# Performance work log

Hardware: AMD Instinct MI355X
Metric: run time of the kernel (lower is better)

## Reference

```python
import jax, jax.numpy as jnp
import numpy as np

H = 128   # d_model / features
N = 32    # kept complex modes (d_state=64 -> 32 conjugate pairs)
B = 8
L = 8192


def setup_inputs() -> dict:
    key = jax.random.key(0)
    ks = jax.random.split(key, 8)
    x = jax.random.normal(ks[0], (B, H, L), jnp.float32)
    # S4D (diagonal SSM) kernel parameters; channels=2 for bidirectional
    C_re = (jax.random.normal(ks[1], (2, H, N), jnp.float32) * (0.5 ** 0.5))
    C_im = (jax.random.normal(ks[2], (2, H, N), jnp.float32) * (0.5 ** 0.5))
    log_A_real = jnp.log(0.5 * jnp.ones((H, N), jnp.float32))          # S4D-Lin init
    A_imag = jnp.tile(np.pi * jnp.arange(N, dtype=jnp.float32), (H, 1))
    # log_dt uniform in [log(1e-3), log(1e-1)]
    u = jax.random.uniform(ks[3], (H,), jnp.float32)
    log_dt = u * (np.log(0.1) - np.log(0.001)) + np.log(0.001)
    D = jax.random.normal(ks[4], (H,), jnp.float32)                    # skip term
    W_pw = jax.random.normal(ks[5], (H, H), jnp.float32) / np.sqrt(H)  # 1x1 conv weight (out, in)
    gamma = jnp.ones((H,), jnp.float32)
    beta = jnp.zeros((H,), jnp.float32)
    return {"x": x, "C_re": C_re, "C_im": C_im, "log_A_real": log_A_real,
            "A_imag": A_imag, "log_dt": log_dt, "D": D, "W_pw": W_pw,
            "gamma": gamma, "beta": beta}


def reference(x, C_re, C_im, log_A_real, A_imag, log_dt, D, W_pw, gamma, beta):
    Lx = x.shape[-1]
    # ---- S4D SSM kernel via Vandermonde (ZOH discretization) ----
    A = -jnp.exp(log_A_real) + 1j * A_imag                 # (H, N) complex
    dt = jnp.exp(log_dt)[:, None]                          # (H, 1)
    dtA = A * dt                                           # (H, N)
    C = C_re + 1j * C_im                                   # (2, H, N)
    Kc = C * ((jnp.exp(dtA) - 1.0) / A)                    # (2, H, N)
    vand = jnp.exp(dtA[:, :, None] * jnp.arange(Lx))       # (H, N, L)
    k = 2.0 * jnp.einsum('chn,hnl->chl', Kc, vand).real    # (2, H, L)
    # ---- bidirectional: causal half + anticausal (flipped) half ----
    k_full = (jnp.pad(k[0], ((0, 0), (0, Lx)))
              + jnp.pad(k[1][:, ::-1], ((0, 0), (Lx, 0))))  # (H, 2L)
    # ---- FFT convolution ----
    n = 2 * Lx
    y = jnp.fft.irfft(jnp.fft.rfft(x, n=n) * jnp.fft.rfft(k_full, n=n), n=n)[..., :Lx]
    y = y + x * D[:, None]                                 # skip connection
    y = jax.nn.gelu(y, approximate=False)                  # FFTConv default activation
    # ---- pointwise 1x1 conv (no bias) ----
    y = jnp.einsum('bhl,oh->bol', y, W_pw)
    # ---- BatchNorm1d (training-mode batch statistics) ----
    mean = jnp.mean(y, axis=(0, 2), keepdims=True)
    var = jnp.var(y, axis=(0, 2), keepdims=True)
    y = (y - mean) * jax.lax.rsqrt(var + 1e-5) * gamma[:, None] + beta[:, None]
    # ---- ELU + residual (dropout p=0) ----
    return jax.nn.elu(y) + x
```

## Files before the change

### kernel.cpp

```cpp
#include <hip/hip_runtime.h>
#include <math.h>

#define HCH   128
#define NMODE 32
#define BB    8
#define LLEN  8192
#define LC    256
#define CCH   (LLEN / LC)
#define ROWS  (BB * HCH)

typedef unsigned int uint;
typedef _Float16 f16x8 __attribute__((ext_vector_type(8)));
typedef float    f32x4 __attribute__((ext_vector_type(4)));

static __device__ __forceinline__ uint pk2(float a, float b) {
    union { _Float16 h[2]; uint u; } v;
    v.h[0] = (_Float16)a; v.h[1] = (_Float16)b;
    return v.u;
}

__device__ __forceinline__ float gelu_f(float y) {
    float z = fabsf(y) * 0.7071067811865476f;
    float p = fmaf(z, 0.078108f, 0.000972f);
    p = fmaf(z, p, 0.230389f);
    p = fmaf(z, p, 0.278393f);
    p = fmaf(z, p, 1.0f);
    float p2 = p * p;
    float p4 = p2 * p2;
    float er = 1.f - __builtin_amdgcn_rcpf(p4);
    float s  = copysignf(er, y);
    return 0.5f * y * (1.f + s);
}

#define DPP_ADD(v, ctrl) { int _t = __builtin_amdgcn_update_dpp(0, __float_as_int(v), \
                             (ctrl), 0xF, 0xF, true); (v) += __int_as_float(_t); }

__global__ __launch_bounds__(256) void k_prep(const float* __restrict__ C_re,
                                              const float* __restrict__ C_im,
                                              const float* __restrict__ logA,
                                              const float* __restrict__ Aim,
                                              const float* __restrict__ logdt,
                                              _Float16* __restrict__ aT,
                                              _Float16* __restrict__ eT,
                                              float* __restrict__ Pw,
                                              float* __restrict__ stats) {
    __shared__ float2 PL[32 * 257];
    __shared__ float4 G01[32];
    __shared__ float4 HG[32];
    __shared__ float2 WL[32];
    __shared__ float k0L[256], k1L[256];
    int tid  = threadIdx.x;
    int h    = blockIdx.x >> 1;
    int half = blockIdx.x & 1;
    if (blockIdx.x == 0) stats[tid] = 0.f;
    if (tid < 32) {
        int n = tid, idx = h * 32 + n;
        float ar = expf(logA[idx]);
        float ai = Aim[idx];
        float dt = expf(logdt[h]);
        float dre = -ar * dt, dim = ai * dt;
        float er = expf(dre);
        float wr = er * cosf(dim), wi = er * sinf(dim);
        WL[n] = (float2){wr, wi};
        if (half == 0) {
            float eL = expf(dre * 256.f);
            Pw[idx]        = eL * cosf(dim * 256.f);
            Pw[4096 + idx] = eL * sinf(dim * 256.f);
        }
        float den  = ar * ar + ai * ai;
        float numr = -(wr - 1.f) * ar + wi * ai;
        float numi = -wi * ar - (wr - 1.f) * ai;
        float Kr = numr / den, Ki = numi / den;
        float c0r = C_re[idx],        c0i = C_im[idx];
        float c1r = C_re[4096 + idx], c1i = C_im[4096 + idx];
        float g0r = 2.f * (c0r * Kr - c0i * Ki), g0i = 2.f * (c0r * Ki + c0i * Kr);
        float g1r = 2.f * (c1r * Kr - c1i * Ki);
        float g1i = 2.f * (c1r * Ki + c1i * Kr);
        G01[n] = (float4){g0r, g0i, g1r, g1i};
        HG[n]  = (float4){g0r * wr - g0i * wi, g0r * wi + g0i * wr, g1r, g1i};
    }
    __syncthreads();
    {
        int n = tid & 31, tg = tid >> 5;
        float2 w = WL[n];
        float w2r = w.x * w.x - w.y * w.y,   w2i = 2.f * w.x * w.y;
        float w4r = w2r * w2r - w2i * w2i,   w4i = 2.f * w2r * w2i;
        float w8r = w4r * w4r - w4i * w4i,   w8i = 2.f * w4r * w4i;
        float pr = (tg & 1) ? w.x : 1.f;
        float pi = (tg & 1) ? w.y : 0.f;
        if (tg & 2) { float t2 = pr * w2r - pi * w2i; pi = pr * w2i + pi * w2r; pr = t2; }
        if (tg & 4) { float t4 = pr * w4r - pi * w4i; pi = pr * w4i + pi * w4r; pr = t4; }
        float2* row = &PL[n * 257];
        #pragma unroll
        for (int j = 0; j < 32; j++) {
            row[tg + 8 * j] = (float2){pr, pi};
            float tr = pr * w8r - pi * w8i; pi = pr * w8i + pi * w8r; pr = tr;
        }
    }
    __syncthreads();
    {
        int tau = tid;
        float s0 = 0.f, s1 = 0.f;
        #pragma unroll
        for (int n = 0; n < 32; n++) {
            float2 p = PL[n * 257 + tau];
            float4 g = G01[n];
            s0 += g.x * p.x - g.y * p.y;
            s1 += g.z * p.x - g.w * p.y;
        }
        k0L[tau] = s0; k1L[tau] = s1;
    }
    __syncthreads();
    #pragma unroll 4
    for (int i = 0; i < 64; i++) {
        int idx = i * 256 + tid;
        int t  = half * 128 + (idx >> 7);
        int sp = (idx & 127) << 1;
        float v0 = (sp     <= t) ? k0L[t - sp]     : k1L[sp - t - 1];
        float v1 = (sp + 1 <= t) ? k0L[t - sp - 1] : k1L[sp - t];
        *(uint*)&aT[((size_t)(h * 256 + t)) * 384 + sp] = pk2(v0, v1);
    }
    #pragma unroll 4
    for (int i = 0; i < 16; i++) {
        int idx = i * 256 + tid;
        int n = idx & 31;
        int t = half * 128 + (idx >> 5);
        float2 pt = PL[n * 257 + t];
        float2 pu = PL[n * 257 + 255 - t];
        float4 hg = HG[n];
        size_t rb = ((size_t)(h * 256 + t)) * 384;
        *(uint*)&aT[rb + 256 + 2 * n] = pk2(hg.x * pt.x - hg.y * pt.y,
                                            -(hg.x * pt.y + hg.y * pt.x));
        *(uint*)&aT[rb + 320 + 2 * n] = pk2(hg.z * pu.x - hg.w * pu.y,
                                            -(hg.z * pu.y + hg.w * pu.x));
    }
    #pragma unroll 4
    for (int i = 0; i < 16; i++) {
        int idx = i * 256 + tid;
        int n = idx >> 7;
        int s = half * 128 + (idx & 127);
        float2 ps = PL[n * 257 + s];
        float2 pu = PL[n * 257 + 255 - s];
        size_t base = (size_t)h * 128 * 256;
        eT[base + (size_t)(2 * n) * 256 + s]      = (_Float16)pu.x;
        eT[base + (size_t)(2 * n + 1) * 256 + s]  = (_Float16)pu.y;
        eT[base + (size_t)(64 + 2 * n) * 256 + s] = (_Float16)ps.x;
        eT[base + (size_t)(65 + 2 * n) * 256 + s] = (_Float16)ps.y;
    }
}

__global__ __launch_bounds__(256, 2) void k_states_g(const float* __restrict__ x,
                                                     const _Float16* __restrict__ eT,
                                                     float* __restrict__ S_end) {
    __shared__ _Float16 At[128 * 40];
    __shared__ _Float16 Bt[128 * 40];
    int tid = threadIdx.x;
    int bid = blockIdx.x;
    int h = bid >> 1, mt = bid & 1;
    int wave = tid >> 6, lane = tid & 63;
    int wm = wave >> 1, wn = wave & 1;
    int lrow = lane & 15, quad = lane >> 4;
    int koff = quad * 8;
    f32x4 acc[4][4];
    #pragma unroll
    for (int a = 0; a < 4; a++)
        #pragma unroll
        for (int b = 0; b < 4; b++) acc[a][b] = (f32x4){0.f, 0.f, 0.f, 0.f};

    for (int kk = 0; kk < 256; kk += 32) {
        __syncthreads();
        #pragma unroll
        for (int i = 0; i < 4; i++) {
            int idx = tid + i * 256;
            int r = idx >> 3, seg = idx & 7;
            int bc = mt * 128 + r;
            const float* xp = x + (((size_t)((bc >> 5) * HCH + h)) << 13) + ((bc & 31) << 8) + kk + seg * 4;
            float4 v = *(const float4*)xp;
            uint2 o; o.x = pk2(v.x, v.y); o.y = pk2(v.z, v.w);
            *(uint2*)&At[r * 40 + seg * 4] = o;
        }
        #pragma unroll
        for (int i = 0; i < 2; i++) {
            int idx = tid + i * 256;
            int r = idx >> 2, sg = idx & 3;
            uint4 v = *(const uint4*)(eT + ((size_t)(h * 128 + r)) * 256 + kk + sg * 8);
            *(uint4*)&Bt[r * 40 + sg * 8] = v;
        }
        __syncthreads();
        f16x8 a[4], b[4];
        #pragma unroll
        for (int f = 0; f < 4; f++) {
            a[f] = *(const f16x8*)&At[(wm * 64 + f * 16 + lrow) * 40 + koff];
            b[f] = *(const f16x8*)&Bt[(wn * 64 + f * 16 + lrow) * 40 + koff];
        }
        #pragma unroll
        for (int fi = 0; fi < 4; fi++)
            #pragma unroll
            for (int fj = 0; fj < 4; fj++)
                acc[fi][fj] = __builtin_amdgcn_mfma_f32_16x16x32_f16(a[fi], b[fj], acc[fi][fj], 0, 0, 0);
    }
    #pragma unroll
    for (int fi = 0; fi < 4; fi++) {
        #pragma unroll
        for (int fj = 0; fj < 4; fj++) {
            int srow = wn * 64 + fj * 16 + lrow;
            #pragma unroll
            for (int rg = 0; rg < 4; rg++) {
                int bc = mt * 128 + wm * 64 + fi * 16 + quad * 4 + rg;
                S_end[((size_t)(h * 256 + bc)) * 128 + srow] = acc[fi][fj][rg];
            }
        }
    }
}

__global__ void k_carries(const float* __restrict__ S_end, const float* __restrict__ Pw,
                          _Float16* __restrict__ carr) {
    int i = blockIdx.x * 256 + threadIdx.x;
    int n = i & 31; int d = (i >> 5) & 1; int row = i >> 6;
    int h = row & (HCH - 1), b = row >> 7;
    int pi = h * NMODE + n;
    float wLr = Pw[pi], wLi = Pw[4096 + pi];
    int srow = d * 64 + 2 * n;
    float cr = 0.f, ci = 0.f;
    if (d == 0) {
        for (int c = 0; c < CCH; c++) {
            size_t base = ((size_t)(h * 256 + b * 32 + c)) * 128 + srow;
            carr[base] = (_Float16)cr; carr[base + 1] = (_Float16)ci;
            float sr = S_end[base], si = S_end[base + 1];
            float nr = fmaf(wLr, cr, -wLi * ci) + sr;
            float ni = fmaf(wLi, cr,  wLr * ci) + si;
            cr = nr; ci = ni;
        }
    } else {
        for (int c = CCH - 1; c >= 0; c--) {
            size_t base = ((size_t)(h * 256 + b * 32 + c)) * 128 + srow;
            carr[base] = (_Float16)cr; carr[base + 1] = (_Float16)ci;
            float sr = S_end[base], si = S_end[base + 1];
            float nr = fmaf(wLr, cr, -wLi * ci) + sr;
            float ni = fmaf(wLi, cr,  wLr * ci) + si;
            cr = nr; ci = ni;
        }
    }
}

__global__ __launch_bounds__(256, 2) void k_conv_g(const float* __restrict__ x,
                                                   const _Float16* __restrict__ aT,
                                                   const _Float16* __restrict__ carr,
                                                   const float* __restrict__ D,
                                                   _Float16* __restrict__ Yg) {
    __shared__ _Float16 At[128 * 40];
    __shared__ _Float16 Bt[128 * 40];
    int tid = threadIdx.x;
    int bid = blockIdx.x;
    int h = bid >> 2, mt = (bid >> 1) & 1, nt = bid & 1;
    int wave = tid >> 6, lane = tid & 63;
    int wm = wave >> 1, wn = wave & 1;
    int lrow = lane & 15, quad = lane >> 4;
    int koff = quad * 8;
    f32x4 acc[4][4];
    #pragma unroll
    for (int a = 0; a < 4; a++)
        #pragma unroll
        for (int b = 0; b < 4; b++) acc[a][b] = (f32x4){0.f, 0.f, 0.f, 0.f};

    for (int kk = 0; kk < 384; kk += 32) {
        __syncthreads();
        if (kk < 256) {
            #pragma unroll
            for (int i = 0; i < 4; i++) {
                int idx = tid + i * 256;
                int r = idx >> 3, seg = idx & 7;
                int bc = mt * 128 + r;
                const float* xp = x + (((size_t)((bc >> 5) * HCH + h)) << 13) + ((bc & 31) << 8) + kk + seg * 4;
                float4 v = *(const float4*)xp;
                uint2 o; o.x = pk2(v.x, v.y); o.y = pk2(v.z, v.w);
                *(uint2*)&At[r * 40 + seg * 4] = o;
            }
        } else {
            #pragma unroll
            for (int i = 0; i < 2; i++) {
                int idx = tid + i * 256;
                int r = idx >> 2, sg = idx & 3;
                int bc = mt * 128 + r;
                uint4 v = *(const uint4*)(carr + ((size_t)(h * 256 + bc)) * 128 + (kk - 256) + sg * 8);
                *(uint4*)&At[r * 40 + sg * 8] = v;
            }
        }
        #pragma unroll
        for (int i = 0; i < 2; i++) {
            int idx = tid + i * 256;
            int r = idx >> 2, sg = idx & 3;
            int t = nt * 128 + r;
            uint4 v = *(const uint4*)(aT + ((size_t)(h * 256 + t)) * 384 + kk + sg * 8);
            *(uint4*)&Bt[r * 40 + sg * 8] = v;
        }
        __syncthreads();
        f16x8 a[4], b[4];
        #pragma unroll
        for (int f = 0; f < 4; f++) {
            a[f] = *(const f16x8*)&At[(wm * 64 + f * 16 + lrow) * 40 + koff];
            b[f] = *(const f16x8*)&Bt[(wn * 64 + f * 16 + lrow) * 40 + koff];
        }
        #pragma unroll
        for (int fi = 0; fi < 4; fi++)
            #pragma unroll
            for (int fj = 0; fj < 4; fj++)
                acc[fi][fj] = __builtin_amdgcn_mfma_f32_16x16x32_f16(a[fi], b[fj], acc[fi][fj], 0, 0, 0);
    }
    float Dh = D[h];
    #pragma unroll
    for (int fi = 0; fi < 4; fi++) {
        #pragma unroll
        for (int fj = 0; fj < 4; fj++) {
            int t = nt * 128 + wn * 64 + fj * 16 + lrow;
            #pragma unroll
            for (int rg = 0; rg < 4; rg++) {
                int bc = mt * 128 + wm * 64 + fi * 16 + quad * 4 + rg;
                size_t base = (((size_t)((bc >> 5) * HCH + h)) << 13) + ((bc & 31) << 8) + t;
                float xv = x[base];
                float yv = acc[fi][fj][rg] + Dh * xv;
                Yg[base] = (_Float16)gelu_f(yv);
            }
        }
    }
}

__global__ __launch_bounds__(256, 2) void k_pointwise(const _Float16* __restrict__ Yg,
                                                      const float* __restrict__ W,
                                                      float* __restrict__ z,
                                                      float* __restrict__ stats) {
    __shared__ _Float16 Wt[128 * 40];
    __shared__ _Float16 Yt[128 * 40];
    int tid = threadIdx.x;
    int b  = blockIdx.x >> 6;
    int l0 = (blockIdx.x & 63) << 7;
    int wave = tid >> 6, lane = tid & 63;
    int wm = wave >> 1, wn = wave & 1;
    int lrow = lane & 15, quad = lane >> 4;
    int koff = quad * 8;
    f32x4 acc[4][4];
    #pragma unroll
    for (int a = 0; a < 4; a++)
        #pragma unroll
        for (int c = 0; c < 4; c++) acc[a][c] = (f32x4){0.f, 0.f, 0.f, 0.f};

    for (int kk = 0; kk < 128; kk += 32) {
        __syncthreads();
        #pragma unroll
        for (int i = 0; i < 4; i++) {
            int idx = tid + i * 256;
            int r = idx >> 3, seg = idx & 7;
            float4 v = *(const float4*)(W + r * HCH + kk + seg * 4);
            uint2 o2; o2.x = pk2(v.x, v.y); o2.y = pk2(v.z, v.w);
            *(uint2*)&Wt[r * 40 + seg * 4] = o2;
        }
        #pragma unroll
        for (int i = 0; i < 2; i++) {
            int idx = tid + i * 256;
            int hh = idx & 31, lg = idx >> 5;
            uint4 v = *(const uint4*)(Yg + (((size_t)(b * HCH + kk + hh)) << 13) + l0 + lg * 8);
            const _Float16* hv = (const _Float16*)&v;
            #pragma unroll
            for (int j = 0; j < 8; j++)
                Yt[(lg * 8 + j) * 40 + hh] = hv[j];
        }
        __syncthreads();
        f16x8 a[4], bf[4];
        #pragma unroll
        for (int f = 0; f < 4; f++) {
            a[f]  = *(const f16x8*)&Wt[(wm * 64 + f * 16 + lrow) * 40 + koff];
            bf[f] = *(const f16x8*)&Yt[(wn * 64 + f * 16 + lrow) * 40 + koff];
        }
        #pragma unroll
        for (int fi = 0; fi < 4; fi++)
            #pragma unroll
            for (int fj = 0; fj < 4; fj++)
                acc[fi][fj] = __builtin_amdgcn_mfma_f32_16x16x32_f16(a[fi], bf[fj], acc[fi][fj], 0, 0, 0);
    }
    #pragma unroll
    for (int fi = 0; fi < 4; fi++) {
        #pragma unroll
        for (int fj = 0; fj < 4; fj++) {
            int l = l0 + wn * 64 + fj * 16 + lrow;
            #pragma unroll
            for (int rg = 0; rg < 4; rg++) {
                int o = wm * 64 + fi * 16 + quad * 4 + rg;
                z[(((size_t)(b * HCH + o)) << 13) + l] = acc[fi][fj][rg];
            }
        }
    }
    __syncthreads();
    float* Ls = (float*)Wt;
    #pragma unroll
    for (int fi = 0; fi < 4; fi++) {
        #pragma unroll
        for (int rg = 0; rg < 4; rg++) {
            float s = 0.f, q = 0.f;
            #pragma unroll
            for (int fj = 0; fj < 4; fj++) {
                float v = acc[fi][fj][rg];
                s += v; q = fmaf(v, v, q);
            }
            DPP_ADD(s, 0xB1); DPP_ADD(s, 0x4E); DPP_ADD(s, 0x141); DPP_ADD(s, 0x140);
            DPP_ADD(q, 0xB1); DPP_ADD(q, 0x4E); DPP_ADD(q, 0x141); DPP_ADD(q, 0x140);
            if (lrow == 0) {
                int olo = fi * 16 + quad * 4 + rg;
                Ls[wave * 64 + olo]       = s;
                Ls[256 + wave * 64 + olo] = q;
            }
        }
    }
    __syncthreads();
    if (tid < HCH) {
        int wmn = tid >> 6;
        int olo = tid & 63;
        float s = Ls[(wmn * 2) * 64 + olo] + Ls[(wmn * 2 + 1) * 64 + olo];
        float q = Ls[256 + (wmn * 2) * 64 + olo] + Ls[256 + (wmn * 2 + 1) * 64 + olo];
        atomicAdd(&stats[tid], s);
        atomicAdd(&stats[HCH + tid], q);
    }
}

__global__ __launch_bounds__(256) void k_final(const float* __restrict__ z,
                                               const float* __restrict__ x,
                                               const float* __restrict__ stats,
                                               const float* __restrict__ gamma,
                                               const float* __restrict__ beta,
                                               float* __restrict__ out) {
    size_t i4 = (size_t)blockIdx.x * 256 + threadIdx.x;
    if (i4 >= (size_t)BB * HCH * LLEN / 4) return;
    size_t flat = i4 * 4;
    int o = (int)((flat / LLEN) & (HCH - 1));
    const float inv_cnt = 1.f / (float)(BB * LLEN);
    float m   = stats[o] * inv_cnt;
    float var = stats[HCH + o] * inv_cnt - m * m;
    float rs  = rsqrtf(var + 1e-5f);
    float ga  = gamma[o] * rs;
    float bt  = beta[o] - m * ga;
    float4 zv = ((const float4*)z)[i4];
    float4 xv = ((const float4*)x)[i4];
    float4 r;
    { float t = fmaf(zv.x, ga, bt); float e = t > 0.f ? t : (__expf(t) - 1.f); r.x = e + xv.x; }
    { float t = fmaf(zv.y, ga, bt); float e = t > 0.f ? t : (__expf(t) - 1.f); r.y = e + xv.y; }
    { float t = fmaf(zv.z, ga, bt); float e = t > 0.f ? t : (__expf(t) - 1.f); r.z = e + xv.z; }
    { float t = fmaf(zv.w, ga, bt); float e = t > 0.f ? t : (__expf(t) - 1.f); r.w = e + xv.w; }
    ((float4*)out)[i4] = r;
}

extern "C" void kernel_launch(void* const* d_in, const int* in_sizes, int n_in,
                              void* d_out, int out_size, void* d_ws, size_t ws_size,
                              hipStream_t stream) {
    const float* x     = (const float*)d_in[0];
    const float* C_re  = (const float*)d_in[1];
    const float* C_im  = (const float*)d_in[2];
    const float* logA  = (const float*)d_in[3];
    const float* Aim   = (const float*)d_in[4];
    const float* logdt = (const float*)d_in[5];
    const float* D     = (const float*)d_in[6];
    const float* W     = (const float*)d_in[7];
    const float* gamma = (const float*)d_in[8];
    const float* beta  = (const float*)d_in[9];

    float* ws = (float*)d_ws;
    _Float16* eT    = (_Float16*)ws;
    float*    S_end = ws + 2097152;
    _Float16* Yg    = (_Float16*)ws;
    float*    zbuf  = ws + 8388608;
    _Float16* aT    = (_Float16*)zbuf;
    _Float16* carr  = (_Float16*)(ws + 16777216);
    float*    Pw    = ws + 16777216 + 2097152;
    float*    stats = Pw + 8192;
    float*    out   = (float*)d_out;

    k_prep     <<<256,  256, 0, stream>>>(C_re, C_im, logA, Aim, logdt, aT, eT, Pw, stats);
    k_states_g <<<256,  256, 0, stream>>>(x, eT, S_end);
    k_carries  <<<256,  256, 0, stream>>>(S_end, Pw, carr);
    k_conv_g   <<<512,  256, 0, stream>>>(x, aT, carr, D, Yg);
    k_pointwise<<<512,  256, 0, stream>>>(Yg, W, zbuf, stats);
    k_final    <<<8192, 256, 0, stream>>>(zbuf, x, stats, gamma, beta, out);
}
```

Measured before the change: 187.9 us.

## Double-buffer GEMM tiles, stage fp16 copies of x and W, store z as fp16

The states kernel now writes an fp16 copy of x, which the conv kernel reads in place of re-converting fp32 x. k_prep pre-converts W to fp16, and the pointwise kernel keeps W fragments in registers. All three MFMA kernels switch to register-prefetched double-buffered LDS tiles with one barrier per k-step, and block indices are remapped so blocks sharing a channel land on the same XCD. The intermediate z is stored as fp16 and k_final processes 8 elements per thread, which halves z traffic at the cost of some precision in the BatchNorm input and stats.

```diff
diff --git a/kernel.cpp b/kernel.cpp
--- a/kernel.cpp
+++ b/kernel.cpp
@@ -40,8 +40,10 @@
                                               const float* __restrict__ logA,
                                               const float* __restrict__ Aim,
                                               const float* __restrict__ logdt,
+                                              const float* __restrict__ W,
                                               _Float16* __restrict__ aT,
                                               _Float16* __restrict__ eT,
+                                              _Float16* __restrict__ Wh,
                                               float* __restrict__ Pw,
                                               float* __restrict__ stats) {
     __shared__ float2 PL[32 * 257];
@@ -53,6 +55,7 @@
     int h    = blockIdx.x >> 1;
     int half = blockIdx.x & 1;
     if (blockIdx.x == 0) stats[tid] = 0.f;
+    if (half == 0 && tid < 128) Wh[h * 128 + tid] = (_Float16)W[h * 128 + tid];
     if (tid < 32) {
         int n = tid, idx = h * 32 + n;
         float ar = expf(logA[idx]);
@@ -151,12 +154,13 @@
 
 __global__ __launch_bounds__(256, 2) void k_states_g(const float* __restrict__ x,
                                                      const _Float16* __restrict__ eT,
-                                                     float* __restrict__ S_end) {
-    __shared__ _Float16 At[128 * 40];
-    __shared__ _Float16 Bt[128 * 40];
+                                                     float* __restrict__ S_end,
+                                                     _Float16* __restrict__ xh) {
+    __shared__ _Float16 At[2][128 * 40];
+    __shared__ _Float16 Bt[2][128 * 40];
     int tid = threadIdx.x;
-    int bid = blockIdx.x;
-    int h = bid >> 1, mt = bid & 1;
+    int xcd = blockIdx.x & 7, slot = blockIdx.x >> 3;
+    int h = xcd * 16 + (slot >> 1), mt = slot & 1;
     int wave = tid >> 6, lane = tid & 63;
     int wm = wave >> 1, wn = wave & 1;
     int lrow = lane & 15, quad = lane >> 4;
@@ -167,37 +171,43 @@
         #pragma unroll
         for (int b = 0; b < 4; b++) acc[a][b] = (f32x4){0.f, 0.f, 0.f, 0.f};
 
-    for (int kk = 0; kk < 256; kk += 32) {
-        __syncthreads();
-        #pragma unroll
-        for (int i = 0; i < 4; i++) {
-            int idx = tid + i * 256;
-            int r = idx >> 3, seg = idx & 7;
-            int bc = mt * 128 + r;
-            const float* xp = x + (((size_t)((bc >> 5) * HCH + h)) << 13) + ((bc & 31) << 8) + kk + seg * 4;
-            float4 v = *(const float4*)xp;
-            uint2 o; o.x = pk2(v.x, v.y); o.y = pk2(v.z, v.w);
-            *(uint2*)&At[r * 40 + seg * 4] = o;
-        }
-        #pragma unroll
-        for (int i = 0; i < 2; i++) {
-            int idx = tid + i * 256;
-            int r = idx >> 2, sg = idx & 3;
-            uint4 v = *(const uint4*)(eT + ((size_t)(h * 128 + r)) * 256 + kk + sg * 8);
-            *(uint4*)&Bt[r * 40 + sg * 8] = v;
-        }
-        __syncthreads();
+    const int chA = tid >> 3, segA = tid & 7;
+    const size_t xbase = (((size_t)(mt * 4) * HCH + h) << 13) + (chA << 8) + segA * 4;
+    const int rB = tid >> 2, sgB = tid & 3;
+
+    float4 ar[4]; uint4 br[2];
+    #define LOADA_S(kk) { _Pragma("unroll") for (int i = 0; i < 4; i++) \
+        ar[i] = *(const float4*)(x + xbase + ((size_t)i << 20) + (kk)); }
+    #define LOADB_S(kk) { _Pragma("unroll") for (int i = 0; i < 2; i++) \
+        br[i] = *(const uint4*)(eT + ((size_t)(h * 128 + rB + 64 * i)) * 256 + (kk) + sgB * 8); }
+    #define WRITE_S(buf, kk) { _Pragma("unroll") for (int i = 0; i < 4; i++) { \
+            uint2 o; o.x = pk2(ar[i].x, ar[i].y); o.y = pk2(ar[i].z, ar[i].w); \
+            *(uint2*)&At[buf][(chA + 32 * i) * 40 + segA * 4] = o; \
+            *(uint2*)&xh[xbase + ((size_t)i << 20) + (kk)] = o; } \
+        _Pragma("unroll") for (int i = 0; i < 2; i++) \
+            *(uint4*)&Bt[buf][(rB + 64 * i) * 40 + sgB * 8] = br[i]; }
+
+    LOADA_S(0); LOADB_S(0);
+    WRITE_S(0, 0);
+    __syncthreads();
+    for (int kt = 0; kt < 8; kt++) {
+        int cur = kt & 1;
+        if (kt < 7) { LOADA_S((kt + 1) * 32); LOADB_S((kt + 1) * 32); }
         f16x8 a[4], b[4];
         #pragma unroll
         for (int f = 0; f < 4; f++) {
-            a[f] = *(const f16x8*)&At[(wm * 64 + f * 16 + lrow) * 40 + koff];
-            b[f] = *(const f16x8*)&Bt[(wn * 64 + f * 16 + lrow) * 40 + koff];
+            a[f] = *(const f16x8*)&At[cur][(wm * 64 + f * 16 + lrow) * 40 + koff];
+            b[f] = *(const f16x8*)&Bt[cur][(wn * 64 + f * 16 + lrow) * 40 + koff];
         }
         #pragma unroll
         for (int fi = 0; fi < 4; fi++)
             #pragma unroll
             for (int fj = 0; fj < 4; fj++)
                 acc[fi][fj] = __builtin_amdgcn_mfma_f32_16x16x32_f16(a[fi], b[fj], acc[fi][fj], 0, 0, 0);
+        if (kt < 7) {
+            WRITE_S(cur ^ 1, (kt + 1) * 32);
+            __syncthreads();
+        }
     }
     #pragma unroll
     for (int fi = 0; fi < 4; fi++) {
@@ -211,6 +221,9 @@
             }
         }
     }
+    #undef LOADA_S
+    #undef LOADB_S
+    #undef WRITE_S
 }
 
 __global__ void k_carries(const float* __restrict__ S_end, const float* __restrict__ Pw,
@@ -243,16 +256,18 @@
     }
 }
 
-__global__ __launch_bounds__(256, 2) void k_conv_g(const float* __restrict__ x,
+__global__ __launch_bounds__(256, 2) void k_conv_g(const _Float16* __restrict__ xh,
                                                    const _Float16* __restrict__ aT,
                                                    const _Float16* __restrict__ carr,
                                                    const float* __restrict__ D,
                                                    _Float16* __restrict__ Yg) {
-    __shared__ _Float16 At[128 * 40];
-    __shared__ _Float16 Bt[128 * 40];
+    __shared__ _Float16 At[2][128 * 40];
+    __shared__ _Float16 Bt[2][128 * 40];
     int tid = threadIdx.x;
-    int bid = blockIdx.x;
-    int h = bid >> 2, mt = (bid >> 1) & 1, nt = bid & 1;
+    int xcd = blockIdx.x & 7, slot = blockIdx.x >> 3;
+    int p = xcd * 32 + (slot >> 1);
+    int mt = slot & 1;
+    int h = p >> 1, nt = p & 1;
     int wave = tid >> 6, lane = tid & 63;
     int wm = wave >> 1, wn = wave & 1;
     int lrow = lane & 15, quad = lane >> 4;
@@ -263,49 +278,41 @@
         #pragma unroll
         for (int b = 0; b < 4; b++) acc[a][b] = (f32x4){0.f, 0.f, 0.f, 0.f};
 
-    for (int kk = 0; kk < 384; kk += 32) {
-        __syncthreads();
-        if (kk < 256) {
-            #pragma unroll
-            for (int i = 0; i < 4; i++) {
-                int idx = tid + i * 256;
-                int r = idx >> 3, seg = idx & 7;
-                int bc = mt * 128 + r;
-                const float* xp = x + (((size_t)((bc >> 5) * HCH + h)) << 13) + ((bc & 31) << 8) + kk + seg * 4;
-                float4 v = *(const float4*)xp;
-                uint2 o; o.x = pk2(v.x, v.y); o.y = pk2(v.z, v.w);
-                *(uint2*)&At[r * 40 + seg * 4] = o;
-            }
-        } else {
-            #pragma unroll
-            for (int i = 0; i < 2; i++) {
-                int idx = tid + i * 256;
-                int r = idx >> 2, sg = idx & 3;
-                int bc = mt * 128 + r;
-                uint4 v = *(const uint4*)(carr + ((size_t)(h * 256 + bc)) * 128 + (kk - 256) + sg * 8);
-                *(uint4*)&At[r * 40 + sg * 8] = v;
-            }
-        }
-        #pragma unroll
-        for (int i = 0; i < 2; i++) {
-            int idx = tid + i * 256;
-            int r = idx >> 2, sg = idx & 3;
-            int t = nt * 128 + r;
-            uint4 v = *(const uint4*)(aT + ((size_t)(h * 256 + t)) * 384 + kk + sg * 8);
-            *(uint4*)&Bt[r * 40 + sg * 8] = v;
-        }
-        __syncthreads();
+    const int rS = tid >> 2, sgS = tid & 3;
+
+    uint4 a_r[2], b_r[2];
+    #define LOADA_C(kk) { _Pragma("unroll") for (int i = 0; i < 2; i++) { \
+            int bc = mt * 128 + rS + 64 * i; \
+            a_r[i] = ((kk) < 256) \
+              ? *(const uint4*)(xh + (((size_t)((bc >> 5) * HCH + h)) << 13) + ((bc & 31) << 8) + (kk) + sgS * 8) \
+              : *(const uint4*)(carr + ((size_t)(h * 256 + bc)) * 128 + ((kk) - 256) + sgS * 8); } }
+    #define LOADB_C(kk) { _Pragma("unroll") for (int i = 0; i < 2; i++) \
+        b_r[i] = *(const uint4*)(aT + ((size_t)(h * 256 + nt * 128 + rS + 64 * i)) * 384 + (kk) + sgS * 8); }
+    #define WRITE_C(buf) { _Pragma("unroll") for (int i = 0; i < 2; i++) { \
+            *(uint4*)&At[buf][(rS + 64 * i) * 40 + sgS * 8] = a_r[i]; \
+            *(uint4*)&Bt[buf][(rS + 64 * i) * 40 + sgS * 8] = b_r[i]; } }
+
+    LOADA_C(0); LOADB_C(0);
+    WRITE_C(0);
+    __syncthreads();
+    for (int kt = 0; kt < 12; kt++) {
+        int cur = kt & 1;
+        if (kt < 11) { LOADA_C((kt + 1) * 32); LOADB_C((kt + 1) * 32); }
         f16x8 a[4], b[4];
         #pragma unroll
         for (int f = 0; f < 4; f++) {
-            a[f] = *(const f16x8*)&At[(wm * 64 + f * 16 + lrow) * 40 + koff];
-            b[f] = *(const f16x8*)&Bt[(wn * 64 + f * 16 + lrow) * 40 + koff];
+            a[f] = *(const f16x8*)&At[cur][(wm * 64 + f * 16 + lrow) * 40 + koff];
+            b[f] = *(const f16x8*)&Bt[cur][(wn * 64 + f * 16 + lrow) * 40 + koff];
         }
         #pragma unroll
         for (int fi = 0; fi < 4; fi++)
             #pragma unroll
             for (int fj = 0; fj < 4; fj++)
                 acc[fi][fj] = __builtin_amdgcn_mfma_f32_16x16x32_f16(a[fi], b[fj], acc[fi][fj], 0, 0, 0);
+        if (kt < 11) {
+            WRITE_C(cur ^ 1);
+            __syncthreads();
+        }
     }
     float Dh = D[h];
     #pragma unroll
@@ -317,20 +324,23 @@
             for (int rg = 0; rg < 4; rg++) {
                 int bc = mt * 128 + wm * 64 + fi * 16 + quad * 4 + rg;
                 size_t base = (((size_t)((bc >> 5) * HCH + h)) << 13) + ((bc & 31) << 8) + t;
-                float xv = x[base];
+                float xv = (float)xh[base];
                 float yv = acc[fi][fj][rg] + Dh * xv;
                 Yg[base] = (_Float16)gelu_f(yv);
             }
         }
     }
+    #undef LOADA_C
+    #undef LOADB_C
+    #undef WRITE_C
 }
 
 __global__ __launch_bounds__(256, 2) void k_pointwise(const _Float16* __restrict__ Yg,
-                                                      const float* __restrict__ W,
-                                                      float* __restrict__ z,
+                                                      const _Float16* __restrict__ Wh,
+                                                      _Float16* __restrict__ z,
                                                       float* __restrict__ stats) {
-    __shared__ _Float16 Wt[128 * 40];
-    __shared__ _Float16 Yt[128 * 40];
+    __shared__ _Float16 Yt[2][128 * 40];
+    __shared__ float Ls[512];
     int tid = threadIdx.x;
     int b  = blockIdx.x >> 6;
     int l0 = (blockIdx.x & 63) << 7;
@@ -344,38 +354,42 @@
         #pragma unroll
         for (int c = 0; c < 4; c++) acc[a][c] = (f32x4){0.f, 0.f, 0.f, 0.f};
 
-    for (int kk = 0; kk < 128; kk += 32) {
-        __syncthreads();
-        #pragma unroll
-        for (int i = 0; i < 4; i++) {
-            int idx = tid + i * 256;
-            int r = idx >> 3, seg = idx & 7;
-            float4 v = *(const float4*)(W + r * HCH + kk + seg * 4);
-            uint2 o2; o2.x = pk2(v.x, v.y); o2.y = pk2(v.z, v.w);
-            *(uint2*)&Wt[r * 40 + seg * 4] = o2;
-        }
-        #pragma unroll
-        for (int i = 0; i < 2; i++) {
-            int idx = tid + i * 256;
-            int hh = idx & 31, lg = idx >> 5;
-            uint4 v = *(const uint4*)(Yg + (((size_t)(b * HCH + kk + hh)) << 13) + l0 + lg * 8);
-            const _Float16* hv = (const _Float16*)&v;
-            #pragma unroll
-            for (int j = 0; j < 8; j++)
-                Yt[(lg * 8 + j) * 40 + hh] = hv[j];
-        }
-        __syncthreads();
-        f16x8 a[4], bf[4];
-        #pragma unroll
-        for (int f = 0; f < 4; f++) {
-            a[f]  = *(const f16x8*)&Wt[(wm * 64 + f * 16 + lrow) * 40 + koff];
-            bf[f] = *(const f16x8*)&Yt[(wn * 64 + f * 16 + lrow) * 40 + koff];
-        }
+    f16x8 a[4][4];
+    #pragma unroll
+    for (int ks = 0; ks < 4; ks++)
+        #pragma unroll
+        for (int f = 0; f < 4; f++)
+            a[ks][f] = *(const f16x8*)(Wh + (wm * 64 + f * 16 + lrow) * HCH + ks * 32 + koff);
+
+    const int hhS = tid & 31;
+    const int lgbase = tid >> 5;
+    uint4 yv[2];
+    #define LOADY(kk) { _Pragma("unroll") for (int i = 0; i < 2; i++) \
+        yv[i] = *(const uint4*)(Yg + (((size_t)(b * HCH + (kk) + hhS)) << 13) + l0 + (lgbase + 8 * i) * 8); }
+    #define WRITEY(buf) { _Pragma("unroll") for (int i = 0; i < 2; i++) { \
+            const _Float16* hv = (const _Float16*)&yv[i]; \
+            _Pragma("unroll") for (int j = 0; j < 8; j++) \
+                Yt[buf][((lgbase + 8 * i) * 8 + j) * 40 + hhS] = hv[j]; } }
+
+    LOADY(0);
+    WRITEY(0);
+    __syncthreads();
+    for (int kt = 0; kt < 4; kt++) {
+        int cur = kt & 1;
+        if (kt < 3) LOADY((kt + 1) * 32);
+        f16x8 bf[4];
+        #pragma unroll
+        for (int f = 0; f < 4; f++)
+            bf[f] = *(const f16x8*)&Yt[cur][(wn * 64 + f * 16 + lrow) * 40 + koff];
         #pragma unroll
         for (int fi = 0; fi < 4; fi++)
             #pragma unroll
             for (int fj = 0; fj < 4; fj++)
-                acc[fi][fj] = __builtin_amdgcn_mfma_f32_16x16x32_f16(a[fi], bf[fj], acc[fi][fj], 0, 0, 0);
+                acc[fi][fj] = __builtin_amdgcn_mfma_f32_16x16x32_f16(a[kt][fi], bf[fj], acc[fi][fj], 0, 0, 0);
+        if (kt < 3) {
+            WRITEY(cur ^ 1);
+            __syncthreads();
+        }
     }
     #pragma unroll
     for (int fi = 0; fi < 4; fi++) {
@@ -385,12 +399,10 @@
             #pragma unroll
             for (int rg = 0; rg < 4; rg++) {
                 int o = wm * 64 + fi * 16 + quad * 4 + rg;
-                z[(((size_t)(b * HCH + o)) << 13) + l] = acc[fi][fj][rg];
+                z[(((size_t)(b * HCH + o)) << 13) + l] = (_Float16)acc[fi][fj][rg];
             }
         }
     }
-    __syncthreads();
-    float* Ls = (float*)Wt;
     #pragma unroll
     for (int fi = 0; fi < 4; fi++) {
         #pragma unroll
@@ -419,32 +431,39 @@
         atomicAdd(&stats[tid], s);
         atomicAdd(&stats[HCH + tid], q);
     }
-}
-
-__global__ __launch_bounds__(256) void k_final(const float* __restrict__ z,
+    #undef LOADY
+    #undef WRITEY
+}
+
+__global__ __launch_bounds__(256) void k_final(const _Float16* __restrict__ z,
                                                const float* __restrict__ x,
                                                const float* __restrict__ stats,
                                                const float* __restrict__ gamma,
                                                const float* __restrict__ beta,
                                                float* __restrict__ out) {
-    size_t i4 = (size_t)blockIdx.x * 256 + threadIdx.x;
-    if (i4 >= (size_t)BB * HCH * LLEN / 4) return;
-    size_t flat = i4 * 4;
-    int o = (int)((flat / LLEN) & (HCH - 1));
+    size_t i8 = (size_t)blockIdx.x * 256 + threadIdx.x;
+    int o = (int)((i8 >> 10) & (HCH - 1));
     const float inv_cnt = 1.f / (float)(BB * LLEN);
     float m   = stats[o] * inv_cnt;
     float var = stats[HCH + o] * inv_cnt - m * m;
     float rs  = rsqrtf(var + 1e-5f);
     float ga  = gamma[o] * rs;
     float bt  = beta[o] - m * ga;
-    float4 zv = ((const float4*)z)[i4];
-    float4 xv = ((const float4*)x)[i4];
-    float4 r;
-    { float t = fmaf(zv.x, ga, bt); float e = t > 0.f ? t : (__expf(t) - 1.f); r.x = e + xv.x; }
-    { float t = fmaf(zv.y, ga, bt); float e = t > 0.f ? t : (__expf(t) - 1.f); r.y = e + xv.y; }
-    { float t = fmaf(zv.z, ga, bt); float e = t > 0.f ? t : (__expf(t) - 1.f); r.z = e + xv.z; }
-    { float t = fmaf(zv.w, ga, bt); float e = t > 0.f ? t : (__expf(t) - 1.f); r.w = e + xv.w; }
-    ((float4*)out)[i4] = r;
+    uint4 zv = ((const uint4*)z)[i8];
+    const _Float16* zh = (const _Float16*)&zv;
+    float4 xa = ((const float4*)x)[2 * i8];
+    float4 xb = ((const float4*)x)[2 * i8 + 1];
+    float4 ra, rb;
+    { float t = fmaf((float)zh[0], ga, bt); float e = t > 0.f ? t : (__expf(t) - 1.f); ra.x = e + xa.x; }
+    { float t = fmaf((float)zh[1], ga, bt); float e = t > 0.f ? t : (__expf(t) - 1.f); ra.y = e + xa.y; }
+    { float t = fmaf((float)zh[2], ga, bt); float e = t > 0.f ? t : (__expf(t) - 1.f); ra.z = e + xa.z; }
+    { float t = fmaf((float)zh[3], ga, bt); float e = t > 0.f ? t : (__expf(t) - 1.f); ra.w = e + xa.w; }
+    { float t = fmaf((float)zh[4], ga, bt); float e = t > 0.f ? t : (__expf(t) - 1.f); rb.x = e + xb.x; }
+    { float t = fmaf((float)zh[5], ga, bt); float e = t > 0.f ? t : (__expf(t) - 1.f); rb.y = e + xb.y; }
+    { float t = fmaf((float)zh[6], ga, bt); float e = t > 0.f ? t : (__expf(t) - 1.f); rb.z = e + xb.z; }
+    { float t = fmaf((float)zh[7], ga, bt); float e = t > 0.f ? t : (__expf(t) - 1.f); rb.w = e + xb.w; }
+    ((float4*)out)[2 * i8]     = ra;
+    ((float4*)out)[2 * i8 + 1] = rb;
 }
 
 extern "C" void kernel_launch(void* const* d_in, const int* in_sizes, int n_in,
@@ -465,17 +484,19 @@
     _Float16* eT    = (_Float16*)ws;
     float*    S_end = ws + 2097152;
     _Float16* Yg    = (_Float16*)ws;
-    float*    zbuf  = ws + 8388608;
-    _Float16* aT    = (_Float16*)zbuf;
+    _Float16* aT    = (_Float16*)(ws + 8388608);
+    _Float16* zf    = (_Float16*)(ws + 8388608);
     _Float16* carr  = (_Float16*)(ws + 16777216);
     float*    Pw    = ws + 16777216 + 2097152;
     float*    stats = Pw + 8192;
+    _Float16* Wh    = (_Float16*)(ws + 18882816);
+    _Float16* xh    = (_Float16*)(ws + 18891008);
     float*    out   = (float*)d_out;
 
-    k_prep     <<<256,  256, 0, stream>>>(C_re, C_im, logA, Aim, logdt, aT, eT, Pw, stats);
-    k_states_g <<<256,  256, 0, stream>>>(x, eT, S_end);
+    k_prep     <<<256,  256, 0, stream>>>(C_re, C_im, logA, Aim, logdt, W, aT, eT, Wh, Pw, stats);
+    k_states_g <<<256,  256, 0, stream>>>(x, eT, S_end, xh);
     k_carries  <<<256,  256, 0, stream>>>(S_end, Pw, carr);
-    k_conv_g   <<<512,  256, 0, stream>>>(x, aT, carr, D, Yg);
-    k_pointwise<<<512,  256, 0, stream>>>(Yg, W, zbuf, stats);
-    k_final    <<<8192, 256, 0, stream>>>(zbuf, x, stats, gamma, beta, out);
-}
+    k_conv_g   <<<512,  256, 0, stream>>>(xh, aT, carr, D, Yg);
+    k_pointwise<<<512,  256, 0, stream>>>(Yg, Wh, zf, stats);
+    k_final    <<<4096, 256, 0, stream>>>(zf, x, stats, gamma, beta, out);
+}
```

Measured after the change: 182.0 us. -3.2%, faster.
